# Optimization experiments

Measured on AMD Instinct MI355X. Metric: run time of the kernel, lower is better.

## Reference

```python
import jax, jax.numpy as jnp
import numpy as np
from jax import lax

B, S, F, I, D, K, V = 8, 4096, 256, 512, 4, 7, 256  # batch, seq, features, intermediate, depth, kernel, classes


def setup_inputs() -> dict:
    key = jax.random.key(0)
    ks = jax.random.split(key, 7)

    def nrm(k, shape, fan_in):
        return jax.random.normal(k, shape, jnp.float32) / np.float32(np.sqrt(fan_in))

    return {
        "inp": jax.random.randint(ks[0], (B, S), 0, V),
        "emb": nrm(ks[1], (V, 2 * F), F),
        "w0": nrm(ks[2], (D, 3 * I, F, 1), F),          # 1x1 gating conv, features -> 3*intermediate
        "w1": nrm(ks[3], (D, 3 * I, I, K), I * K),       # causal conv, intermediate -> 3*intermediate
        "w2": nrm(ks[4], (D, F, I, 1), I),               # 1x1 conv, intermediate -> features
        "out_w": nrm(ks[5], (V, 2 * F, 1), 2 * F),
        "out_b": jnp.zeros((V,), jnp.float32),
    }


def mish(x):
    return x * jnp.tanh(jax.nn.softplus(x))


def conv1x1(x, w):
    # x: [B, C, S], w: [O, C, 1] -> [B, O, S]
    return jnp.einsum('bcs,oc->bos', x, w[..., 0])


def causal_conv(x, w):
    # x: [B, C, S], w: [O, C, K]; left-pad with K-1 zeros for causality
    k = w.shape[-1]
    xp = jnp.pad(x, ((0, 0), (0, 0), (k - 1, 0)))
    return lax.conv_general_dilated(xp, w, (1,), 'VALID',
                                    dimension_numbers=('NCH', 'OIH', 'NCH'))


def lin_attn(v, divisor):
    # v: [B, 3I, S]; cumsum-normalized linear attention: cumsum(depth)/t * scale + shift
    depth, scale, shift = jnp.split(v, 3, axis=1)
    return jnp.cumsum(depth, axis=-1) / divisor * scale + shift


def cell(x, w0, w1, w2, divisor):
    v = lin_attn(mish(conv1x1(x, w0)), divisor)     # [B, I, S]
    v = lin_attn(mish(causal_conv(v, w1)), divisor) # [B, I, S]
    return conv1x1(v, w2)                            # [B, F, S]


def reference(inp, emb, w0, w1, w2, out_w, out_b):
    divisor = jnp.arange(1, S + 1, dtype=jnp.float32)[None, None, :]  # [1,1,S]
    e = jnp.transpose(emb[inp], (0, 2, 1))  # [B, 2F, S]
    x0, x1 = jnp.split(e, 2, axis=1)
    # reversible residual stack: (x0, x1) -> (x1, x0 + cell(x1))
    for d in range(D):
        x0, x1 = x1, x0 + cell(x1, w0[d], w1[d], w2[d], divisor)
    out = jnp.concatenate([x0, x1], axis=1)  # [B, 2F, S]
    return conv1x1(out, out_w) + out_b[None, :, None]  # [B, V, S]
```

## Files before the change

kernel.cpp:

```cpp
#include <hip/hip_runtime.h>
#include <hip/hip_bf16.h>

#define B_ 8
#define S_ 4096
#define F_ 256
#define I_ 512
#define D_ 4
#define K_ 7
#define V_ 256
#define I3_ 1536
#define KE_ 3584
#define VR_ (S_ + 8)

using bf16 = __hip_bfloat16;
typedef __bf16 bf16x8 __attribute__((ext_vector_type(8)));
typedef float  f32x4  __attribute__((ext_vector_type(4)));

#define LDS_PTR(p) ((__attribute__((address_space(3))) void*)(p))
#define GLB_PTR(p) ((const __attribute__((address_space(1))) void*)(p))

#define BARR_()  __builtin_amdgcn_s_barrier()
#define WLGKM_() asm volatile("s_waitcnt lgkmcnt(0)" ::: "memory")
#define WVM0_()  asm volatile("s_waitcnt vmcnt(0)" ::: "memory")

__device__ __forceinline__ float mishf(float x) {
    float u = expf(fminf(x, 30.0f));
    float t = u * (u + 2.0f);
    return x * (t / (t + 2.0f));
}

__device__ __forceinline__ float loadw(const void* p, size_t i, int isbf) {
    return isbf ? __bfloat162float(((const bf16*)p)[i]) : ((const float*)p)[i];
}

__device__ __forceinline__ __bf16 tobf(float x) {
    bf16 h = __float2bfloat16(x);
    return *(__bf16*)&h;
}

__device__ __forceinline__ float bf2f(__bf16 h) {
    unsigned short u = __builtin_bit_cast(unsigned short, h);
    unsigned int x = (unsigned int)u << 16;
    return __builtin_bit_cast(float, x);
}

__global__ __launch_bounds__(256)
void detect_kernel(int* __restrict__ flag, const unsigned short* __restrict__ p)
{
    __shared__ int sh[256];
    int cnt = 0;
    for (int j = threadIdx.x; j < 16384; j += 256) {
        unsigned int e = (p[j] >> 7) & 0xffu;
        if (e >= 132u) cnt++;
    }
    sh[threadIdx.x] = cnt;
    __syncthreads();
    for (int s = 128; s > 0; s >>= 1) {
        if ((int)threadIdx.x < s) sh[threadIdx.x] += sh[threadIdx.x + s];
        __syncthreads();
    }
    if (threadIdx.x == 0) flag[0] = (sh[0] == 0) ? 1 : 0;
}

__global__ __launch_bounds__(256)
void embed_kernel(float* __restrict__ x0, float* __restrict__ x1,
                  const int* __restrict__ inp, const void* __restrict__ emb,
                  const int* __restrict__ flag)
{
    const int isbf = flag[0];
    size_t idx = (size_t)blockIdx.x * 256 + threadIdx.x;
    int s = (int)(idx % S_);
    int f = (int)((idx / S_) % F_);
    int b = (int)(idx / ((size_t)S_ * F_));
    int tok = inp[b * S_ + s];
    x0[idx] = loadw(emb, (size_t)tok * (2 * F_) + f, isbf);
    x1[idx] = loadw(emb, (size_t)tok * (2 * F_) + F_ + f, isbf);
}

__global__ __launch_bounds__(256)
void zeropad_kernel(bf16* __restrict__ vbt, int nslice)
{
    int i = blockIdx.x * 256 + threadIdx.x;
    if (i < nslice * 6 * I_) {
        int z = i / (6 * I_), off = i % (6 * I_);
        vbt[(size_t)z * VR_ * I_ + off] = __float2bfloat16(0.0f);
    }
}

__global__ __launch_bounds__(256)
void wprep_kernel(bf16* __restrict__ wexp, bf16* __restrict__ wb0,
                  bf16* __restrict__ wb2, const void* __restrict__ w1,
                  const void* __restrict__ w0, const void* __restrict__ w2,
                  size_t o1w, size_t o0w, size_t o2w, const int* __restrict__ flag)
{
    const int isbf = flag[0];
    int idx = blockIdx.x * 256 + threadIdx.x;
    if (idx < I3_ * I_) {
        int c = idx & 511, o = idx >> 9;
        const size_t base = o1w + ((size_t)o * 512 + c) * 7;
        float vals[7];
        #pragma unroll
        for (int k = 0; k < 7; ++k) vals[k] = loadw(w1, base + k, isbf);
        #pragma unroll
        for (int k = 0; k < 7; ++k)
            wexp[(size_t)o * KE_ + (k << 9) + c] = __float2bfloat16(vals[k]);
    } else if (idx < I3_ * I_ + I3_ * F_) {
        int i = idx - I3_ * I_;
        wb0[i] = __float2bfloat16(loadw(w0, o0w + i, isbf));
    } else if (idx < I3_ * I_ + I3_ * F_ + F_ * I_) {
        int i = idx - I3_ * I_ - I3_ * F_;
        wb2[i] = __float2bfloat16(loadw(w2, o2w + i, isbf));
    }
}

__global__ __launch_bounds__(256)
void scan_kernel(bf16* __restrict__ vout, const float* __restrict__ td,
                 const bf16* __restrict__ tb)
{
    const int z = blockIdx.y;
    const int i = blockIdx.x;
    td   += (size_t)z * I_ * S_;
    tb   += (size_t)z * 2 * I_ * S_;
    vout += (size_t)z * I_ * S_;
    const float* dp = td + (size_t)i * S_;
    const bf16* scp = tb + (size_t)i * S_;
    const bf16* shp = tb + (size_t)(I_ + i) * S_;
    bf16* op = vout + (size_t)i * S_;
    const int tid = threadIdx.x;
    const int base = tid * 16;

    float md[16];
    float lsum = 0.f;
    #pragma unroll
    for (int q = 0; q < 4; ++q) {
        float4 dv = *(const float4*)(dp + base + q * 4);
        #pragma unroll
        for (int j = 0; j < 4; ++j) {
            float m = (&dv.x)[j];
            md[q * 4 + j] = m;
            lsum += m;
        }
    }
    float ssum = lsum;
    #pragma unroll
    for (int off = 1; off < 64; off <<= 1) {
        float nv = __shfl_up(ssum, off, 64);
        if ((tid & 63) >= off) ssum += nv;
    }
    __shared__ float wtot[4];
    const int wid = tid >> 6, lane = tid & 63;
    if (lane == 63) wtot[wid] = ssum;
    __syncthreads();
    float excl = ssum - lsum;
    #pragma unroll
    for (int wq = 0; wq < 3; ++wq)
        if (wq < wid) excl += wtot[wq];

    bf16x8 scv0 = *(const bf16x8*)(const void*)(scp + base);
    bf16x8 scv1 = *(const bf16x8*)(const void*)(scp + base + 8);
    bf16x8 shv0 = *(const bf16x8*)(const void*)(shp + base);
    bf16x8 shv1 = *(const bf16x8*)(const void*)(shp + base + 8);

    float run = excl;
    bf16x8 o0v, o1v;
    #pragma unroll
    for (int e = 0; e < 16; ++e) {
        run += md[e];
        float sdiv = (float)(base + e + 1);
        float sc = bf2f((e < 8) ? scv0[e] : scv1[e - 8]);
        float sh = bf2f((e < 8) ? shv0[e] : shv1[e - 8]);
        float ov = run / sdiv * sc + sh;
        if (e < 8) o0v[e] = tobf(ov);
        else       o1v[e - 8] = tobf(ov);
    }
    *(bf16x8*)(void*)(op + base) = o0v;
    *(bf16x8*)(void*)(op + base + 8) = o1v;
}

__global__ __launch_bounds__(256)
void trans_kernel(bf16* __restrict__ dst, size_t dzstr,
                  const float* __restrict__ src, size_t szstr, int C)
{
    __shared__ __align__(16) bf16 lt[64][72];
    const int z = blockIdx.z;
    dst += (size_t)z * dzstr;
    src += (size_t)z * szstr;
    const int tid = threadIdx.x;
    const int s0 = blockIdx.x * 64;
    const int c0 = blockIdx.y * 64;
    #pragma unroll
    for (int p = 0; p < 4; ++p) {
        int c = p * 16 + (tid >> 4);
        int sc = (tid & 15) * 4;
        float4 f = *(const float4*)(src + (size_t)(c0 + c) * S_ + s0 + sc);
        #pragma unroll
        for (int j = 0; j < 4; ++j)
            lt[sc + j][c] = __float2bfloat16((&f.x)[j]);
    }
    __syncthreads();
    #pragma unroll
    for (int p = 0; p < 2; ++p) {
        int ch = p * 256 + tid;
        int r = ch >> 3, g = ch & 7;
        *(bf16x8*)(dst + (size_t)(s0 + r) * C + c0 + g * 8) =
            *(const bf16x8*)&lt[r][g * 8];
    }
}

__global__ __launch_bounds__(256)
void transb_kernel(bf16* __restrict__ dst, size_t dzstr,
                   const bf16* __restrict__ src, size_t szstr, int C)
{
    __shared__ __align__(16) bf16 lt[64][72];
    const int z = blockIdx.z;
    dst += (size_t)z * dzstr;
    src += (size_t)z * szstr;
    const int tid = threadIdx.x;
    const int s0 = blockIdx.x * 64;
    const int c0 = blockIdx.y * 64;
    #pragma unroll
    for (int p = 0; p < 2; ++p) {
        int c = p * 32 + (tid >> 3);
        int sc = (tid & 7) * 8;
        bf16x8 v = *(const bf16x8*)(src + (size_t)(c0 + c) * S_ + s0 + sc);
        #pragma unroll
        for (int j = 0; j < 8; ++j)
            *(__bf16*)&lt[sc + j][c] = v[j];
    }
    __syncthreads();
    #pragma unroll
    for (int p = 0; p < 2; ++p) {
        int ch = p * 256 + tid;
        int r = ch >> 3, g = ch & 7;
        *(bf16x8*)(dst + (size_t)(s0 + r) * C + c0 + g * 8) =
            *(const bf16x8*)&lt[r][g * 8];
    }
}

__global__ __launch_bounds__(512, 1)
void gemm192_kernel(float* __restrict__ outd, bf16* __restrict__ outb,
                    const bf16* __restrict__ Aw, int lda,
                    const bf16* __restrict__ Bm, size_t bzstr, int ldb,
                    int Kdim, int conv)
{
    __shared__ __align__(16) bf16 la[2][192][64];
    __shared__ __align__(16) bf16 lb[2][256][64];
    const int tid = threadIdx.x;
    const int s0 = blockIdx.x * 256;
    const int o0 = blockIdx.y * 192;
    const int z  = blockIdx.z;
    outd += (size_t)z * I_ * S_;
    outb += (size_t)z * 2 * I_ * S_;
    Bm   += (size_t)z * bzstr;
    const int wv = tid >> 6, lane = tid & 63;
    const int wr = wv >> 2, wc = wv & 3;
    const int l16 = lane & 15, q = lane >> 4;
    const int srow = lane >> 3;
    const int schunk = (lane & 7) ^ srow;
    const int nKt = Kdim >> 6;

    f32x4 acc[6][4];
    #pragma unroll
    for (int i = 0; i < 6; ++i)
        #pragma unroll
        for (int j = 0; j < 4; ++j)
            #pragma unroll
            for (int r = 0; r < 4; ++r) acc[i][j][r] = 0.f;

#define STAGE_A3(buf, kt) do {                                                \
    const bf16* gpA_ = Aw + (size_t)(o0 + wv * 8 + srow) * lda                \
                          + ((kt) << 6) + (schunk << 3);                      \
    __builtin_amdgcn_global_load_lds(GLB_PTR(gpA_),                           \
        LDS_PTR(&la[buf][wv * 8][0]), 16, 0, 0);                              \
    __builtin_amdgcn_global_load_lds(GLB_PTR(gpA_ + (size_t)64 * lda),        \
        LDS_PTR(&la[buf][64 + wv * 8][0]), 16, 0, 0);                         \
    __builtin_amdgcn_global_load_lds(GLB_PTR(gpA_ + (size_t)128 * lda),       \
        LDS_PTR(&la[buf][128 + wv * 8][0]), 16, 0, 0);                        \
} while (0)

#define STAGE_BL(buf, l, ro, bk) do {                                         \
    const bf16* gpB_ = Bm + (size_t)(s0 + (l) * 64 + wv * 8 + srow + (ro)) * ldb \
                          + (bk) + (schunk << 3);                             \
    __builtin_amdgcn_global_load_lds(GLB_PTR(gpB_),                           \
        LDS_PTR(&lb[buf][(l) * 64 + wv * 8][0]), 16, 0, 0);                   \
} while (0)

#define LDAF6(buf, kk) do {                                                   \
    _Pragma("unroll") for (int i2 = 0; i2 < 6; ++i2) {                        \
        int r_ = wr * 96 + i2 * 16 + l16;                                     \
        af[i2] = *(const bf16x8*)&la[buf][r_][(((kk) * 4 + q) ^ (r_ & 7)) << 3]; \
    }                                                                         \
} while (0)

#define LDBF4(buf, kk) do {                                                   \
    _Pragma("unroll") for (int j2 = 0; j2 < 4; ++j2) {                        \
        int r_ = wc * 64 + j2 * 16 + l16;                                     \
        bfr[j2] = *(const bf16x8*)&lb[buf][r_][(((kk) * 4 + q) ^ (r_ & 7)) << 3]; \
    }                                                                         \
} while (0)

#define MFMA24() do {                                                         \
    __builtin_amdgcn_s_setprio(1);                                            \
    _Pragma("unroll") for (int i2 = 0; i2 < 6; ++i2)                          \
    _Pragma("unroll") for (int j2 = 0; j2 < 4; ++j2)                          \
        acc[i2][j2] = __builtin_amdgcn_mfma_f32_16x16x32_bf16(                \
            af[i2], bfr[j2], acc[i2][j2], 0, 0, 0);                           \
    __builtin_amdgcn_s_setprio(0);                                            \
} while (0)

    STAGE_A3(0, 0);
    STAGE_BL(0, 0, 0, 0); STAGE_BL(0, 1, 0, 0);
    STAGE_BL(0, 2, 0, 0); STAGE_BL(0, 3, 0, 0);
    WVM0_();
    BARR_();

    bf16x8 af[6], bfr[4];
    for (int t = 0; t < nKt; ++t) {
        const int c = t & 1, n = c ^ 1;
        const bool st = (t + 1) < nKt;
        int ro1 = 0, bk1 = (t + 1) << 6;
        if (conv) { ro1 = bk1 >> 9; bk1 &= 511; }
        LDAF6(c, 0); LDBF4(c, 0);
        if (st) {
            STAGE_A3(n, t + 1);
            STAGE_BL(n, 0, ro1, bk1); STAGE_BL(n, 1, ro1, bk1);
            STAGE_BL(n, 2, ro1, bk1); STAGE_BL(n, 3, ro1, bk1);
        }
        BARR_(); WLGKM_();
        MFMA24();
        LDAF6(c, 1); LDBF4(c, 1);
        if (st) WVM0_();
        BARR_(); WLGKM_();
        MFMA24();
    }

    #pragma unroll
    for (int i = 0; i < 6; ++i)
        #pragma unroll
        for (int j = 0; j < 4; ++j) {
            int sg = s0 + wc * 64 + j * 16 + l16;
            #pragma unroll
            for (int r = 0; r < 4; ++r) {
                int og = o0 + wr * 96 + i * 16 + q * 4 + r;
                float v = mishf(acc[i][j][r]);
                if (og < I_) outd[(size_t)og * S_ + sg] = v;
                else outb[(size_t)(og - I_) * S_ + sg] = __float2bfloat16(v);
            }
        }
#undef STAGE_A3
#undef STAGE_BL
#undef LDAF6
#undef LDBF4
#undef MFMA24
}

__global__ __launch_bounds__(512, 1)
void gemm256_kernel(float* __restrict__ outd, bf16* __restrict__ outb,
                    const bf16* __restrict__ Aw, int lda,
                    const bf16* __restrict__ Bm, size_t bzstr, int ldb,
                    int Kdim, int conv)
{
    __shared__ __align__(16) bf16 la[2][256][64];
    __shared__ __align__(16) bf16 lb[2][256][64];
    const int tid = threadIdx.x;
    const int s0 = blockIdx.x * 256;
    const int o0 = blockIdx.y * 256;
    const int z  = blockIdx.z;
    outd += (size_t)z * I_ * S_;
    outb += (size_t)z * 2 * I_ * S_;
    Bm   += (size_t)z * bzstr;
    const int wv = tid >> 6, lane = tid & 63;
    const int wr = wv >> 2, wc = wv & 3;
    const int l16 = lane & 15, q = lane >> 4;
    const int srow = lane >> 3;
    const int schunk = (lane & 7) ^ srow;
    const int nKt = Kdim >> 6;

    f32x4 acc[8][4];
    #pragma unroll
    for (int i = 0; i < 8; ++i)
        #pragma unroll
        for (int j = 0; j < 4; ++j)
            #pragma unroll
            for (int r = 0; r < 4; ++r) acc[i][j][r] = 0.f;

#define STAGE_A4(buf, kt) do {                                                \
    const bf16* gpA_ = Aw + (size_t)(o0 + wv * 8 + srow) * lda                \
                          + ((kt) << 6) + (schunk << 3);                      \
    __builtin_amdgcn_global_load_lds(GLB_PTR(gpA_),                           \
        LDS_PTR(&la[buf][wv * 8][0]), 16, 0, 0);                              \
    __builtin_amdgcn_global_load_lds(GLB_PTR(gpA_ + (size_t)64 * lda),        \
        LDS_PTR(&la[buf][64 + wv * 8][0]), 16, 0, 0);                         \
    __builtin_amdgcn_global_load_lds(GLB_PTR(gpA_ + (size_t)128 * lda),       \
        LDS_PTR(&la[buf][128 + wv * 8][0]), 16, 0, 0);                        \
    __builtin_amdgcn_global_load_lds(GLB_PTR(gpA_ + (size_t)192 * lda),       \
        LDS_PTR(&la[buf][192 + wv * 8][0]), 16, 0, 0);                        \
} while (0)

#define STAGE_BL2(buf, l, ro, bk) do {                                        \
    const bf16* gpB_ = Bm + (size_t)(s0 + (l) * 64 + wv * 8 + srow + (ro)) * ldb \
                          + (bk) + (schunk << 3);                             \
    __builtin_amdgcn_global_load_lds(GLB_PTR(gpB_),                           \
        LDS_PTR(&lb[buf][(l) * 64 + wv * 8][0]), 16, 0, 0);                   \
} while (0)

#define LDAF8(buf, kk) do {                                                   \
    _Pragma("unroll") for (int i2 = 0; i2 < 8; ++i2) {                        \
        int r_ = wr * 128 + i2 * 16 + l16;                                    \
        af[i2] = *(const bf16x8*)&la[buf][r_][(((kk) * 4 + q) ^ (r_ & 7)) << 3]; \
    }                                                                         \
} while (0)

#define LDBF4B(buf, kk) do {                                                  \
    _Pragma("unroll") for (int j2 = 0; j2 < 4; ++j2) {                        \
        int r_ = wc * 64 + j2 * 16 + l16;                                     \
        bfr[j2] = *(const bf16x8*)&lb[buf][r_][(((kk) * 4 + q) ^ (r_ & 7)) << 3]; \
    }                                                                         \
} while (0)

#define MFMA32() do {                                                         \
    __builtin_amdgcn_s_setprio(1);                                            \
    _Pragma("unroll") for (int i2 = 0; i2 < 8; ++i2)                          \
    _Pragma("unroll") for (int j2 = 0; j2 < 4; ++j2)                          \
        acc[i2][j2] = __builtin_amdgcn_mfma_f32_16x16x32_bf16(                \
            af[i2], bfr[j2], acc[i2][j2], 0, 0, 0);                           \
    __builtin_amdgcn_s_setprio(0);                                            \
} while (0)

    STAGE_A4(0, 0);
    STAGE_BL2(0, 0, 0, 0); STAGE_BL2(0, 1, 0, 0);
    STAGE_BL2(0, 2, 0, 0); STAGE_BL2(0, 3, 0, 0);
    WVM0_();
    BARR_();

    bf16x8 af[8], bfr[4];
    for (int t = 0; t < nKt; ++t) {
        const int c = t & 1, n = c ^ 1;
        const bool st = (t + 1) < nKt;
        int ro1 = 0, bk1 = (t + 1) << 6;
        if (conv) { ro1 = bk1 >> 9; bk1 &= 511; }
        LDAF8(c, 0); LDBF4B(c, 0);
        if (st) {
            STAGE_A4(n, t + 1);
            STAGE_BL2(n, 0, ro1, bk1); STAGE_BL2(n, 1, ro1, bk1);
            STAGE_BL2(n, 2, ro1, bk1); STAGE_BL2(n, 3, ro1, bk1);
        }
        BARR_(); WLGKM_();
        MFMA32();
        LDAF8(c, 1); LDBF4B(c, 1);
        if (st) WVM0_();
        BARR_(); WLGKM_();
        MFMA32();
    }

    #pragma unroll
    for (int i = 0; i < 8; ++i)
        #pragma unroll
        for (int j = 0; j < 4; ++j) {
            int sg = s0 + wc * 64 + j * 16 + l16;
            #pragma unroll
            for (int r = 0; r < 4; ++r) {
                int og = o0 + wr * 128 + i * 16 + q * 4 + r;
                float v = mishf(acc[i][j][r]);
                if (og < I_) outd[(size_t)og * S_ + sg] = v;
                else outb[(size_t)(og - I_) * S_ + sg] = __float2bfloat16(v);
            }
        }
#undef STAGE_A4
#undef STAGE_BL2
#undef LDAF8
#undef LDBF4B
#undef MFMA32
}

__global__ __launch_bounds__(256)
void gemm128_kernel(float* __restrict__ out, size_t ozstr,
                    const bf16* __restrict__ Aw, int lda,
                    const bf16* __restrict__ Bm, size_t bzstr, int ldb,
                    int Kdim, int conv, int addres)
{
    __shared__ __align__(16) bf16 la[2][128][64];
    __shared__ __align__(16) bf16 lb[2][128][64];
    const int tid = threadIdx.x;
    const int s0 = blockIdx.x * 128;
    const int o0 = blockIdx.y * 128;
    const int z  = blockIdx.z;
    out += (size_t)z * ozstr;
    Bm  += (size_t)z * bzstr;
    const int wv = tid >> 6, lane = tid & 63;
    const int wo = wv & 1, wsv = wv >> 1;
    const int l16 = lane & 15, q = lane >> 4;
    const int lrow = lane >> 3, lslot = lane & 7;
    const int nKt = Kdim >> 6;

    f32x4 acc[4][4];
    #pragma unroll
    for (int i = 0; i < 4; ++i)
        #pragma unroll
        for (int j = 0; j < 4; ++j)
            #pragma unroll
            for (int r = 0; r < 4; ++r) acc[i][j][r] = 0.f;

#define G128_STAGE(buf, kt) do {                                              \
    int k0_ = (kt) << 6; int roff_ = 0, bk_ = k0_;                            \
    if (conv) { roff_ = k0_ >> 9; bk_ = k0_ & 511; }                          \
    _Pragma("unroll") for (int t_ = 0; t_ < 4; ++t_) {                        \
        int rbase = wv * 32 + t_ * 8;                                         \
        int row = rbase + lrow;                                               \
        int chunk = lslot ^ (row & 7);                                        \
        __builtin_amdgcn_global_load_lds(                                     \
            GLB_PTR(Aw + (size_t)(o0 + row) * lda + k0_ + chunk * 8),         \
            LDS_PTR(&la[buf][rbase][0]), 16, 0, 0);                           \
        __builtin_amdgcn_global_load_lds(                                     \
            GLB_PTR(Bm + (size_t)(s0 + row + roff_) * ldb + bk_ + chunk * 8), \
            LDS_PTR(&lb[buf][rbase][0]), 16, 0, 0);                           \
    }                                                                         \
} while (0)

#define G128_RD(buf, kk) do {                                                 \
    _Pragma("unroll") for (int i = 0; i < 4; ++i) {                           \
        int r = wo * 64 + i * 16 + l16;                                       \
        af[i] = *(const bf16x8*)&la[buf][r][(((kk) * 4 + q) ^ (r & 7)) * 8];  \
    }                                                                         \
    _Pragma("unroll") for (int j = 0; j < 4; ++j) {                           \
        int r = wsv * 64 + j * 16 + l16;                                      \
        bfr[j] = *(const bf16x8*)&lb[buf][r][(((kk) * 4 + q) ^ (r & 7)) * 8]; \
    }                                                                         \
} while (0)

#define G128_MFMA16() do {                                                    \
    __builtin_amdgcn_s_setprio(1);                                            \
    _Pragma("unroll") for (int i = 0; i < 4; ++i)                             \
    _Pragma("unroll") for (int j = 0; j < 4; ++j)                             \
        acc[i][j] = __builtin_amdgcn_mfma_f32_16x16x32_bf16(                  \
            af[i], bfr[j], acc[i][j], 0, 0, 0);                               \
    __builtin_amdgcn_s_setprio(0);                                            \
} while (0)

    G128_STAGE(0, 0);
    WVM0_();
    BARR_();

    bf16x8 af[4], bfr[4];
    for (int t = 0; t < nKt; ++t) {
        const int c = t & 1, n = c ^ 1;
        const bool st = (t + 1) < nKt;
        G128_RD(c, 0);
        if (st) G128_STAGE(n, t + 1);
        BARR_(); WLGKM_();
        G128_MFMA16();
        G128_RD(c, 1);
        if (st) WVM0_();
        BARR_(); WLGKM_();
        G128_MFMA16();
    }

    #pragma unroll
    for (int i = 0; i < 4; ++i)
        #pragma unroll
        for (int j = 0; j < 4; ++j) {
            int sg = s0 + wsv * 64 + j * 16 + l16;
            #pragma unroll
            for (int r = 0; r < 4; ++r) {
                int og = o0 + wo * 64 + i * 16 + q * 4 + r;
                float v = acc[i][j][r];
                if (addres) v += out[(size_t)og * S_ + sg];
                out[(size_t)og * S_ + sg] = v;
            }
        }
#undef G128_STAGE
#undef G128_RD
#undef G128_MFMA16
}

__global__ __launch_bounds__(256)
void final_kernel(void* __restrict__ out, const float* __restrict__ x0,
                  const float* __restrict__ x1, const void* __restrict__ ow,
                  const void* __restrict__ ob, const int* __restrict__ flag)
{
    __shared__ float wl[16][68];
    __shared__ float xl[16][68];
    const int isbf = flag[0];
    const int tid = threadIdx.x;
    const int tx = tid & 15, ty = tid >> 4;
    const int s0 = blockIdx.x * 64;
    const int o0 = blockIdx.y * 64;
    const int b  = blockIdx.z;
    float acc[4][4] = {};
    for (int c0 = 0; c0 < 2 * F_; c0 += 16) {
        if (isbf) {
            #pragma unroll
            for (int e = tid; e < 1024; e += 256) {
                int k = e & 15, o = e >> 4;
                wl[k][o] = __bfloat162float(((const bf16*)ow)[(size_t)(o0 + o) * (2 * F_) + (c0 + k)]);
            }
        } else {
            #pragma unroll
            for (int e = tid; e < 1024; e += 256) {
                int k = e & 15, o = e >> 4;
                wl[k][o] = ((const float*)ow)[(size_t)(o0 + o) * (2 * F_) + (c0 + k)];
            }
        }
        {
            int r = tid >> 4;
            int qq = (tid & 15) * 4;
            int cr = c0 + r;
            const float* src = (cr < F_) ? (x0 + ((size_t)b * F_ + cr) * S_)
                                         : (x1 + ((size_t)b * F_ + (cr - F_)) * S_);
            *(float4*)&xl[r][qq] = *(const float4*)(src + s0 + qq);
        }
        __syncthreads();
        #pragma unroll
        for (int k = 0; k < 16; ++k) {
            float4 av = *(const float4*)&wl[k][ty * 4];
            float4 bv = *(const float4*)&xl[k][tx * 4];
            #pragma unroll
            for (int i = 0; i < 4; ++i)
                #pragma unroll
                for (int j = 0; j < 4; ++j)
                    acc[i][j] += (&av.x)[i] * (&bv.x)[j];
        }
        __syncthreads();
    }
    #pragma unroll
    for (int i = 0; i < 4; ++i) {
        int o = o0 + ty * 4 + i;
        float bias = loadw(ob, o, isbf);
        size_t outoff = ((size_t)b * V_ + o) * S_ + s0 + tx * 4;
        if (isbf) {
            bf16* po = (bf16*)out + outoff;
            #pragma unroll
            for (int j = 0; j < 4; ++j)
                po[j] = __float2bfloat16(acc[i][j] + bias);
        } else {
            float* po = (float*)out + outoff;
            *(float4*)po = make_float4(acc[i][0] + bias, acc[i][1] + bias,
                                       acc[i][2] + bias, acc[i][3] + bias);
        }
    }
}

extern "C" void kernel_launch(void* const* d_in, const int* in_sizes, int n_in,
                              void* d_out, int out_size, void* d_ws, size_t ws_size,
                              hipStream_t stream)
{
    const int*  inp  = (const int*)d_in[0];
    const void* emb  = d_in[1];
    const void* w0   = d_in[2];
    const void* w1   = d_in[3];
    const void* w2   = d_in[4];
    const void* outw = d_in[5];
    const void* outb = d_in[6];

    const size_t NX = (size_t)B_ * F_ * S_;
    const size_t NIS = (size_t)I_ * S_;
    const size_t VSTR = (size_t)VR_ * I_;

    auto need = [&](int p) -> size_t {
        return 256 + 8 * NX
             + (size_t)4 * p * NIS
             + (size_t)4 * p * NIS
             + (size_t)2 * p * NIS
             + 2 * ((size_t)I3_ * KE_ + (size_t)p * VSTR + (size_t)p * S_ * F_
                    + (size_t)I3_ * F_ + (size_t)F_ * I_);
    };
    int P = 2;
    if (ws_size >= need(8)) P = 8;
    else if (ws_size >= need(4)) P = 4;

    int*   flag = (int*)d_ws;
    float* A  = (float*)d_ws + 64;
    float* Bb = A + NX;
    float* Td = Bb + NX;
    bf16*  Tb = (bf16*)(Td + (size_t)P * NIS);
    bf16*  Vv = Tb + (size_t)P * 2 * NIS;
    bf16*  wexp = Vv + (size_t)P * NIS;
    bf16*  vbt  = wexp + (size_t)I3_ * KE_;
    bf16*  xbt  = vbt + (size_t)P * VSTR;
    bf16*  wb0  = xbt + (size_t)P * S_ * F_;
    bf16*  wb2  = wb0 + (size_t)I3_ * F_;

    detect_kernel<<<1, 256, 0, stream>>>(flag, (const unsigned short*)emb);
    embed_kernel<<<dim3((unsigned)(NX / 256)), 256, 0, stream>>>(A, Bb, inp, emb, flag);
    zeropad_kernel<<<dim3((P * 6 * I_ + 255) / 256), 256, 0, stream>>>(vbt, P);

    const unsigned WPREP_GRID = (I3_ * I_ + I3_ * F_ + F_ * I_ + 255) / 256;
    int swap = 0;
    for (int d = 0; d < D_; ++d) {
        wprep_kernel<<<dim3(WPREP_GRID), 256, 0, stream>>>(
            wexp, wb0, wb2, w1, w0, w2,
            (size_t)d * I3_ * I_ * K_, (size_t)d * I3_ * F_,
            (size_t)d * F_ * I_, flag);
        for (int bp = 0; bp < B_ / P; ++bp) {
            float* x0 = (swap ? Bb : A) + (size_t)(P * bp) * F_ * S_;
            float* x1 = (swap ? A : Bb) + (size_t)(P * bp) * F_ * S_;
            trans_kernel<<<dim3(S_ / 64, F_ / 64, P), 256, 0, stream>>>(
                xbt, (size_t)S_ * F_, x1, (size_t)F_ * S_, F_);
            if (P == 8)
                gemm256_kernel<<<dim3(S_ / 256, I3_ / 256, 8), 512, 0, stream>>>(
                    Td, Tb, wb0, F_, xbt, (size_t)S_ * F_, F_, F_, 0);
            else
                gemm192_kernel<<<dim3(S_ / 256, I3_ / 192, P), 512, 0, stream>>>(
                    Td, Tb, wb0, F_, xbt, (size_t)S_ * F_, F_, F_, 0);
            scan_kernel<<<dim3(I_, P), 256, 0, stream>>>(Vv, Td, Tb);
            transb_kernel<<<dim3(S_ / 64, I_ / 64, P), 256, 0, stream>>>(
                vbt + 6 * I_, VSTR, Vv, NIS, I_);
            if (P == 8)
                gemm256_kernel<<<dim3(S_ / 256, I3_ / 256, 8), 512, 0, stream>>>(
                    Td, Tb, wexp, KE_, vbt, VSTR, I_, KE_, 1);
            else
                gemm192_kernel<<<dim3(S_ / 256, I3_ / 192, P), 512, 0, stream>>>(
                    Td, Tb, wexp, KE_, vbt, VSTR, I_, KE_, 1);
            scan_kernel<<<dim3(I_, P), 256, 0, stream>>>(Vv, Td, Tb);
            transb_kernel<<<dim3(S_ / 64, I_ / 64, P), 256, 0, stream>>>(
                vbt + 6 * I_, VSTR, Vv, NIS, I_);
            gemm128_kernel<<<dim3(S_ / 128, F_ / 128, P), 256, 0, stream>>>(
                x0, (size_t)F_ * S_, wb2, I_, vbt + 6 * I_, VSTR, I_, I_, 0, 1);
        }
        swap ^= 1;
    }
    final_kernel<<<dim3(S_ / 64, V_ / 64, B_), 256, 0, stream>>>(d_out, A, Bb, outw, outb, flag);
    (void)in_sizes; (void)n_in; (void)out_size;
}
```

Before: 2.506 ms.

## Restructure 256x256 GEMM main loop into quadrant-interleaved staged pipeline

Rewrites the big GEMM's K loop to process two K-tiles per iteration. Each 64x64 weight/activation tile is split into half-tiles staged at finer granularity, interleaved with quadrant-sized MFMA batches. Global-to-LDS loads for the next tiles are spread across the compute phases, with partial vmcnt/lgkmcnt waits, so memory traffic overlaps MFMA work instead of sitting behind one full wait per tile. The cost is many more barriers and intricate buffer-reuse ordering, which risks races and requires nKt to be even.

```diff
diff --git a/kernel.cpp b/kernel.cpp
--- a/kernel.cpp
+++ b/kernel.cpp
@@ -21,7 +21,10 @@
 
 #define BARR_()  __builtin_amdgcn_s_barrier()
 #define WLGKM_() asm volatile("s_waitcnt lgkmcnt(0)" ::: "memory")
+#define WLGK8_() asm volatile("s_waitcnt lgkmcnt(8)" ::: "memory")
 #define WVM0_()  asm volatile("s_waitcnt vmcnt(0)" ::: "memory")
+#define WVM6_()  asm volatile("s_waitcnt vmcnt(6)" ::: "memory")
+#define WVM8_()  asm volatile("s_waitcnt vmcnt(8)" ::: "memory")
 
 __device__ __forceinline__ float mishf(float x) {
     float u = expf(fminf(x, 30.0f));
@@ -384,73 +387,109 @@
             #pragma unroll
             for (int r = 0; r < 4; ++r) acc[i][j][r] = 0.f;
 
-#define STAGE_A4(buf, kt) do {                                                \
-    const bf16* gpA_ = Aw + (size_t)(o0 + wv * 8 + srow) * lda                \
+#define STAGE_AH(buf, h, kt) do {                                             \
+    const bf16* gpA_ = Aw + (size_t)(o0 + (h) * 64 + wv * 8 + srow) * lda     \
                           + ((kt) << 6) + (schunk << 3);                      \
     __builtin_amdgcn_global_load_lds(GLB_PTR(gpA_),                           \
-        LDS_PTR(&la[buf][wv * 8][0]), 16, 0, 0);                              \
-    __builtin_amdgcn_global_load_lds(GLB_PTR(gpA_ + (size_t)64 * lda),        \
-        LDS_PTR(&la[buf][64 + wv * 8][0]), 16, 0, 0);                         \
+        LDS_PTR(&la[buf][(h) * 64 + wv * 8][0]), 16, 0, 0);                   \
     __builtin_amdgcn_global_load_lds(GLB_PTR(gpA_ + (size_t)128 * lda),       \
-        LDS_PTR(&la[buf][128 + wv * 8][0]), 16, 0, 0);                        \
-    __builtin_amdgcn_global_load_lds(GLB_PTR(gpA_ + (size_t)192 * lda),       \
-        LDS_PTR(&la[buf][192 + wv * 8][0]), 16, 0, 0);                        \
-} while (0)
-
-#define STAGE_BL2(buf, l, ro, bk) do {                                        \
-    const bf16* gpB_ = Bm + (size_t)(s0 + (l) * 64 + wv * 8 + srow + (ro)) * ldb \
+        LDS_PTR(&la[buf][128 + (h) * 64 + wv * 8][0]), 16, 0, 0);             \
+} while (0)
+
+#define STAGE_BH(buf, h, ro, bk) do {                                         \
+    const int rb_ = (h) * 32 + (wv >> 2) * 64 + (wv & 3) * 8;                 \
+    const bf16* gpB_ = Bm + (size_t)(s0 + rb_ + srow + (ro)) * ldb            \
                           + (bk) + (schunk << 3);                             \
     __builtin_amdgcn_global_load_lds(GLB_PTR(gpB_),                           \
-        LDS_PTR(&lb[buf][(l) * 64 + wv * 8][0]), 16, 0, 0);                   \
-} while (0)
-
-#define LDAF8(buf, kk) do {                                                   \
-    _Pragma("unroll") for (int i2 = 0; i2 < 8; ++i2) {                        \
-        int r_ = wr * 128 + i2 * 16 + l16;                                    \
-        af[i2] = *(const bf16x8*)&la[buf][r_][(((kk) * 4 + q) ^ (r_ & 7)) << 3]; \
+        LDS_PTR(&lb[buf][rb_][0]), 16, 0, 0);                                 \
+    __builtin_amdgcn_global_load_lds(GLB_PTR(gpB_ + (size_t)128 * ldb),       \
+        LDS_PTR(&lb[buf][128 + rb_][0]), 16, 0, 0);                           \
+} while (0)
+
+#define LDAQ(buf, qa) do {                                                    \
+    _Pragma("unroll") for (int i2 = 0; i2 < 4; ++i2)                          \
+    _Pragma("unroll") for (int kk = 0; kk < 2; ++kk) {                        \
+        int r_ = wr * 128 + (qa) * 64 + i2 * 16 + l16;                        \
+        af[i2 * 2 + kk] =                                                     \
+            *(const bf16x8*)&la[buf][r_][((kk * 4 + q) ^ (r_ & 7)) << 3];     \
     }                                                                         \
 } while (0)
 
-#define LDBF4B(buf, kk) do {                                                  \
-    _Pragma("unroll") for (int j2 = 0; j2 < 4; ++j2) {                        \
-        int r_ = wc * 64 + j2 * 16 + l16;                                     \
-        bfr[j2] = *(const bf16x8*)&lb[buf][r_][(((kk) * 4 + q) ^ (r_ & 7)) << 3]; \
+#define LDBQ(dst, buf, qb) do {                                               \
+    _Pragma("unroll") for (int j2 = 0; j2 < 2; ++j2)                          \
+    _Pragma("unroll") for (int kk = 0; kk < 2; ++kk) {                        \
+        int r_ = wc * 64 + (qb) * 32 + j2 * 16 + l16;                         \
+        dst[j2 * 2 + kk] =                                                    \
+            *(const bf16x8*)&lb[buf][r_][((kk * 4 + q) ^ (r_ & 7)) << 3];     \
     }                                                                         \
 } while (0)
 
-#define MFMA32() do {                                                         \
+#define MFMAQ(qa, qb, bfx) do {                                               \
     __builtin_amdgcn_s_setprio(1);                                            \
-    _Pragma("unroll") for (int i2 = 0; i2 < 8; ++i2)                          \
-    _Pragma("unroll") for (int j2 = 0; j2 < 4; ++j2)                          \
-        acc[i2][j2] = __builtin_amdgcn_mfma_f32_16x16x32_bf16(                \
-            af[i2], bfr[j2], acc[i2][j2], 0, 0, 0);                           \
+    _Pragma("unroll") for (int kk = 0; kk < 2; ++kk)                          \
+    _Pragma("unroll") for (int i2 = 0; i2 < 4; ++i2)                          \
+    _Pragma("unroll") for (int j2 = 0; j2 < 2; ++j2)                          \
+        acc[(qa) * 4 + i2][(qb) * 2 + j2] =                                   \
+            __builtin_amdgcn_mfma_f32_16x16x32_bf16(                          \
+                af[i2 * 2 + kk], bfx[j2 * 2 + kk],                            \
+                acc[(qa) * 4 + i2][(qb) * 2 + j2], 0, 0, 0);                  \
     __builtin_amdgcn_s_setprio(0);                                            \
 } while (0)
 
-    STAGE_A4(0, 0);
-    STAGE_BL2(0, 0, 0, 0); STAGE_BL2(0, 1, 0, 0);
-    STAGE_BL2(0, 2, 0, 0); STAGE_BL2(0, 3, 0, 0);
-    WVM0_();
+    STAGE_AH(0, 0, 0); STAGE_AH(0, 1, 0);
+    STAGE_BH(0, 0, 0, 0); STAGE_BH(0, 1, 0, 0);
+    STAGE_AH(1, 0, 1); STAGE_AH(1, 1, 1);
+    STAGE_BH(1, 0, 0, 64); STAGE_BH(1, 1, 0, 64);
+    WVM8_();
     BARR_();
 
-    bf16x8 af[8], bfr[4];
-    for (int t = 0; t < nKt; ++t) {
-        const int c = t & 1, n = c ^ 1;
-        const bool st = (t + 1) < nKt;
-        int ro1 = 0, bk1 = (t + 1) << 6;
-        if (conv) { ro1 = bk1 >> 9; bk1 &= 511; }
-        LDAF8(c, 0); LDBF4B(c, 0);
-        if (st) {
-            STAGE_A4(n, t + 1);
-            STAGE_BL2(n, 0, ro1, bk1); STAGE_BL2(n, 1, ro1, bk1);
-            STAGE_BL2(n, 2, ro1, bk1); STAGE_BL2(n, 3, ro1, bk1);
-        }
+    bf16x8 af[8], bf0[4], bf1[4];
+    for (int t0 = 0; t0 < nKt; t0 += 2) {
+        const bool st2 = (t0 + 2) < nKt;
+        const bool st3 = (t0 + 3) < nKt;
+        int ro2 = 0, bk2 = (t0 + 2) << 6;
+        int ro3 = 0, bk3 = (t0 + 3) << 6;
+        if (conv) { ro2 = bk2 >> 9; bk2 &= 511; ro3 = bk3 >> 9; bk3 &= 511; }
+        LDAQ(0, 0); LDBQ(bf0, 0, 0);
+        if (t0 > 0) STAGE_AH(1, 1, t0 + 1);
+        WLGK8_(); BARR_(); WLGKM_();
+        MFMAQ(0, 0, bf0);
+        BARR_();
+        LDBQ(bf1, 0, 1);
+        if (st2) STAGE_AH(0, 0, t0 + 2);
         BARR_(); WLGKM_();
-        MFMA32();
-        LDAF8(c, 1); LDBF4B(c, 1);
-        if (st) WVM0_();
+        MFMAQ(0, 1, bf1);
+        BARR_();
+        LDAQ(0, 1);
+        if (st2) STAGE_BH(0, 0, ro2, bk2);
         BARR_(); WLGKM_();
-        MFMA32();
+        MFMAQ(1, 1, bf1);
+        BARR_();
+        if (st2) STAGE_BH(0, 1, ro2, bk2);
+        BARR_();
+        MFMAQ(1, 0, bf0);
+        if (st2) { WVM6_(); } else { WVM0_(); }
+        BARR_();
+        LDAQ(1, 0); LDBQ(bf0, 1, 0);
+        if (st2) STAGE_AH(0, 1, t0 + 2);
+        WLGK8_(); BARR_(); WLGKM_();
+        MFMAQ(0, 0, bf0);
+        BARR_();
+        LDBQ(bf1, 1, 1);
+        if (st3) STAGE_AH(1, 0, t0 + 3);
+        BARR_(); WLGKM_();
+        MFMAQ(0, 1, bf1);
+        BARR_();
+        LDAQ(1, 1);
+        if (st3) STAGE_BH(1, 0, ro3, bk3);
+        BARR_(); WLGKM_();
+        MFMAQ(1, 1, bf1);
+        BARR_();
+        if (st3) STAGE_BH(1, 1, ro3, bk3);
+        BARR_();
+        MFMAQ(1, 0, bf0);
+        if (st3) { WVM6_(); } else { WVM0_(); }
+        BARR_();
     }
 
     #pragma unroll
@@ -466,11 +505,11 @@
                 else outb[(size_t)(og - I_) * S_ + sg] = __float2bfloat16(v);
             }
         }
-#undef STAGE_A4
-#undef STAGE_BL2
-#undef LDAF8
-#undef LDBF4B
-#undef MFMA32
+#undef STAGE_AH
+#undef STAGE_BH
+#undef LDAQ
+#undef LDBQ
+#undef MFMAQ
 }
 
 __global__ __launch_bounds__(256)
```

New measurement: 2.508 ms. Within noise of the previous version (+0.1%).
